# Kernel tuning notes

Measured on AMD Instinct MI355X. Metric: run time of the kernel, lower is better.

## Reference

```python
import jax, jax.numpy as jnp
import numpy as np

B, T, D, H = 4, 4096, 1024, 4
DK = D // H
DV = D // H
CH = 64           # chunk_size
C = T // CH


def setup_inputs() -> dict:
    key = jax.random.key(0)
    ks = jax.random.split(key, 10)
    def w(k, shape, fan_in):
        return jax.random.normal(k, shape, jnp.float32) * (fan_in ** -0.5)
    return {
        "x": jax.random.normal(ks[0], (B, T, D), jnp.float32),
        "Wq": w(ks[1], (D, D), D),
        "Wk": w(ks[2], (D, D), D),
        "Wv": w(ks[3], (D, D), D),
        "Wb": w(ks[4], (D, H), D),      # beta projection
        "Wa": w(ks[5], (D, H), D),      # decay-gate projection
        "A_log": jnp.log(jax.random.uniform(ks[6], (H,), jnp.float32, 1.0, 16.0)),
        "dt_bias": jnp.zeros((H,), jnp.float32),
        "Wg": w(ks[7], (D, D), D),      # output-gate projection
        "norm_w": jnp.ones((DV,), jnp.float32),
        "Wo": w(ks[8], (D, D), D),
    }


def _l2norm(x, eps=1e-6):
    return x * jax.lax.rsqrt(jnp.sum(x * x, axis=-1, keepdims=True) + eps)


def _gdn_forward(x, Wq, Wk, Wv, Wb, Wa, A_log, dt_bias, Wg, norm_w, Wo):
    # projections; q/k L2-normalized per head, q scaled by 1/sqrt(dk)
    q = _l2norm((x @ Wq).reshape(B, T, H, DK)) * (DK ** -0.5)
    k = _l2norm((x @ Wk).reshape(B, T, H, DK))
    v = (x @ Wv).reshape(B, T, H, DV)
    beta = jax.nn.sigmoid(x @ Wb)                                        # [B,T,H]
    dec = jnp.exp(-jnp.exp(A_log) * jax.nn.softplus(x @ Wa + dt_bias))   # [B,T,H] in (0,1)

    # gated delta rule recurrence: S_t = dec_t*S_{t-1} + beta_t * k_t (v_t - k_t^T S_{t-1})
    def step(S, t):
        qt, kt, vt, bt, dt = t                    # [B,H,DK],[B,H,DK],[B,H,DV],[B,H],[B,H]
        S = S * dt[..., None, None]               # gated decay of state [B,H,DK,DV]
        pred = jnp.einsum('bhk,bhkv->bhv', kt, S)
        S = S + kt[..., :, None] * (bt[..., None] * (vt - pred))[..., None, :]
        ot = jnp.einsum('bhk,bhkv->bhv', qt, S)
        return S, ot

    def chunk_fn(S, chunk):
        return jax.lax.scan(step, S, chunk)
    chunk_fn = jax.checkpoint(chunk_fn)           # store only chunk-boundary states

    def to_chunks(a):                              # [B,T,...] -> [C,CH,B,H,...]
        a = jnp.moveaxis(a, 1, 0)
        return a.reshape((C, CH) + a.shape[1:])

    xs = tuple(to_chunks(a) for a in (q, k, v, beta, dec))
    S0 = jnp.zeros((B, H, DK, DV), jnp.float32)
    _, o = jax.lax.scan(chunk_fn, S0, xs)         # o: [C,CH,B,H,DV]
    o = jnp.moveaxis(o.reshape(T, B, H, DV), 0, 1)  # [B,T,H,DV]

    # gated RMSNorm + output projection
    gate = (x @ Wg).reshape(B, T, H, DV)
    o = o * jax.lax.rsqrt(jnp.mean(o * o, axis=-1, keepdims=True) + 1e-5) * norm_w
    o = o * jax.nn.silu(gate)
    return o.reshape(B, T, D) @ Wo


def reference(x, Wq, Wk, Wv, Wb, Wa, A_log, dt_bias, Wg, norm_w, Wo):
    return _gdn_forward(x, Wq, Wk, Wv, Wb, Wa, A_log, dt_bias, Wg, norm_w, Wo)
```

## Files before the change

kernel.cpp:

```cpp
#include <hip/hip_runtime.h>

typedef unsigned short u16;
typedef __bf16 bf16x8 __attribute__((ext_vector_type(8)));
typedef u16 u16x8 __attribute__((ext_vector_type(8)));
typedef u16 u16x4 __attribute__((ext_vector_type(4)));
typedef float f32x4 __attribute__((ext_vector_type(4)));

__device__ __forceinline__ float bf2f(u16 v) {
    union { unsigned u; float f; } c; c.u = ((unsigned)v) << 16; return c.f;
}
__device__ __forceinline__ u16 f2bf_h(float f) {
    __bf16 h = (__bf16)f;
    union { __bf16 h; u16 u; } c; c.h = h; return c.u;
}

__device__ __forceinline__ bf16x8 ldfrag(const u16* base, int stride, int row0, int k0, int lane) {
    return *(const bf16x8*)(base + (size_t)(row0 + (lane & 15)) * stride + k0 + (lane >> 4) * 8);
}

__device__ __forceinline__ void block_barrier() {
    __builtin_amdgcn_sched_barrier(0);
    asm volatile("s_waitcnt lgkmcnt(0)");
    __builtin_amdgcn_s_barrier();
    __builtin_amdgcn_sched_barrier(0);
}

__device__ __forceinline__ void gl2lds16(const void* g, void* l) {
    __builtin_amdgcn_global_load_lds(
        (const __attribute__((address_space(1))) unsigned int*)g,
        (__attribute__((address_space(3))) unsigned int*)l, 16, 0, 0);
}

__global__ __launch_bounds__(256) void cvt_kernel(const float* __restrict__ src,
                                                  u16* __restrict__ dst) {
    const long i = ((long)blockIdx.x * 256 + threadIdx.x) * 4;
    f32x4 v = *(const f32x4*)(src + i);
    u16x4 o;
#pragma unroll
    for (int r = 0; r < 4; r++) o[r] = f2bf_h(v[r]);
    *(u16x4*)(dst + i) = o;
}

__global__ __launch_bounds__(256) void transpose5_kernel(const float* __restrict__ s0,
                                                         const float* __restrict__ s1,
                                                         const float* __restrict__ s2,
                                                         const float* __restrict__ s3,
                                                         const float* __restrict__ s4,
                                                         u16* __restrict__ dstBase) {
    __shared__ float tile[32][33];
    const int z = blockIdx.z;
    const float* src = (z == 0) ? s0 : (z == 1) ? s1 : (z == 2) ? s2 : (z == 3) ? s3 : s4;
    u16* dst = dstBase + (size_t)z * 1024 * 1024;
    const int n0 = blockIdx.x * 32, k0 = blockIdx.y * 32;
    const int tx = threadIdx.x, ty = threadIdx.y;
#pragma unroll
    for (int i = 0; i < 32; i += 8)
        tile[ty + i][tx] = src[(long)(k0 + ty + i) * 1024 + n0 + tx];
    __syncthreads();
#pragma unroll
    for (int i = 0; i < 32; i += 8)
        dst[(long)(n0 + ty + i) * 1024 + k0 + tx] = f2bf_h(tile[tx][ty + i]);
}

template <int F32OUT>
__global__ __launch_bounds__(256) void gemm_kernel(const u16* __restrict__ A,
                                                   const u16* __restrict__ BT,
                                                   void* __restrict__ Cv,
                                                   int M, int N, int K, int ldc) {
    __shared__ __attribute__((aligned(16))) u16 As[128][32];
    __shared__ __attribute__((aligned(16))) u16 Bs[128][32];
    const int tid  = threadIdx.x;
    const int lane = tid & 63;
    const int wave = tid >> 6;
    const int wm   = (wave >> 1) * 64;
    const int wn   = (wave & 1) * 64;
    const long m0  = (long)blockIdx.y * 128;
    const long n0  = (long)blockIdx.x * 128;

    const f32x4 zero = {0.f, 0.f, 0.f, 0.f};
    f32x4 acc[4][4];
#pragma unroll
    for (int i = 0; i < 4; i++)
#pragma unroll
        for (int j = 0; j < 4; j++) acc[i][j] = zero;

    const int r0 = tid >> 2;
    const int c0 = (tid & 3) * 8;
    const u16* Ag = A + (m0 + r0) * K + c0;
    const u16* Bg = BT + (n0 + r0) * K + c0;
    u16* AsW  = &As[wave * 16][0];
    u16* AsW2 = &As[wave * 16 + 64][0];
    u16* BsW  = &Bs[wave * 16][0];
    u16* BsW2 = &Bs[wave * 16 + 64][0];

    for (int k0 = 0; k0 < K; k0 += 32) {
        gl2lds16(Ag + k0, AsW);
        gl2lds16(Ag + (long)64 * K + k0, AsW2);
        gl2lds16(Bg + k0, BsW);
        gl2lds16(Bg + (long)64 * K + k0, BsW2);
        __syncthreads();
        const int qk = (lane >> 4) * 8;
        const int mr = lane & 15;
        bf16x8 af[4], bfr[4];
#pragma unroll
        for (int i = 0; i < 4; i++) af[i]  = *(const bf16x8*)(&As[wm + i * 16 + mr][qk]);
#pragma unroll
        for (int j = 0; j < 4; j++) bfr[j] = *(const bf16x8*)(&Bs[wn + j * 16 + mr][qk]);
#pragma unroll
        for (int i = 0; i < 4; i++)
#pragma unroll
            for (int j = 0; j < 4; j++)
                acc[i][j] = __builtin_amdgcn_mfma_f32_16x16x32_bf16(af[i], bfr[j], acc[i][j], 0, 0, 0);
        __syncthreads();
    }

    const int cr = (lane >> 4) * 4;
    const int cc = lane & 15;
#pragma unroll
    for (int i = 0; i < 4; i++) {
#pragma unroll
        for (int j = 0; j < 4; j++) {
            const long m = m0 + wm + i * 16 + cr;
            const long n = n0 + wn + j * 16 + cc;
            if (F32OUT) {
                float* C = (float*)Cv;
#pragma unroll
                for (int r = 0; r < 4; r++) C[(m + r) * ldc + n] = acc[i][j][r];
            } else {
                u16* C = (u16*)Cv;
#pragma unroll
                for (int r = 0; r < 4; r++) C[(m + r) * ldc + n] = f2bf_h(acc[i][j][r]);
            }
        }
    }
}

__global__ __launch_bounds__(1024) void norm_beta_kernel(
    const u16* __restrict__ xb, u16* __restrict__ Y,
    const float* __restrict__ Wb, const float* __restrict__ Wa,
    const float* __restrict__ A_log, const float* __restrict__ dt_bias,
    float* __restrict__ beta, float* __restrict__ dec) {
    const long row = blockIdx.x;
    const int c = threadIdx.x;
    const int h = c >> 8;
    float qv = bf2f(Y[row * 3072 + c]);
    float kv = bf2f(Y[row * 3072 + 1024 + c]);
    float xv = bf2f(xb[row * 1024 + c]);
    float vals[10];
    vals[0] = qv * qv;
    vals[1] = kv * kv;
#pragma unroll
    for (int hh = 0; hh < 4; hh++) vals[2 + hh] = xv * Wb[c * 4 + hh];
#pragma unroll
    for (int hh = 0; hh < 4; hh++) vals[6 + hh] = xv * Wa[c * 4 + hh];
#pragma unroll
    for (int i = 0; i < 10; i++)
        for (int off = 32; off; off >>= 1) vals[i] += __shfl_xor(vals[i], off, 64);

    __shared__ float wred[16][10];
    __shared__ float sQ[4], sK[4];
    const int w = c >> 6;
    if ((c & 63) == 0) {
#pragma unroll
        for (int i = 0; i < 10; i++) wred[w][i] = vals[i];
    }
    __syncthreads();
    if (c < 4) {
        float s = wred[c * 4 + 0][0] + wred[c * 4 + 1][0] + wred[c * 4 + 2][0] + wred[c * 4 + 3][0];
        sQ[c] = rsqrtf(s + 1e-6f) * 0.0625f;
    } else if (c < 8) {
        int hh = c - 4;
        float s = wred[hh * 4 + 0][1] + wred[hh * 4 + 1][1] + wred[hh * 4 + 2][1] + wred[hh * 4 + 3][1];
        sK[hh] = rsqrtf(s + 1e-6f);
    } else if (c < 12) {
        int hh = c - 8;
        float s = 0.f;
        for (int ww = 0; ww < 16; ww++) s += wred[ww][2 + hh];
        beta[row * 4 + hh] = 1.f / (1.f + expf(-s));
    } else if (c < 16) {
        int hh = c - 12;
        float s = 0.f;
        for (int ww = 0; ww < 16; ww++) s += wred[ww][6 + hh];
        float z = s + dt_bias[hh];
        float sp = (z > 0.f) ? (z + log1pf(expf(-z))) : log1pf(expf(z));
        dec[row * 4 + hh] = expf(-expf(A_log[hh]) * sp);
    }
    __syncthreads();
    Y[row * 3072 + c]        = f2bf_h(qv * sQ[h]);
    Y[row * 3072 + 1024 + c] = f2bf_h(kv * sK[h]);
}

__global__ __launch_bounds__(256) void prep_kernel(const u16* __restrict__ Y,
                                                   const float* __restrict__ beta,
                                                   const float* __restrict__ dec,
                                                   u16* __restrict__ Tg,
                                                   u16* __restrict__ Mg,
                                                   float* __restrict__ sfg) {
    __shared__ __attribute__((aligned(16))) u16 lds[38400];
    __shared__ float sf[320];
    u16* KS  = lds;
    u16* QS  = lds + 16896;
    u16* AM  = lds + 33792;
    u16* Tm  = lds;
    u16* AMT = lds + 4608;
    u16* MP  = lds + 9216;
    u16* MPT = lds + 13824;

    const int bx = blockIdx.x;
    const int bh = bx >> 6, c = bx & 63;
    const int b = bh >> 2, h = bh & 3;
    const int tid = threadIdx.x, lane = tid & 63, wv = tid >> 6;
    const int quad = lane >> 4, l15 = lane & 15;
    const int tld = tid >> 2, seg = tid & 3;
    const long bt0 = (long)b * 4096 + c * 64;
    u16* Tc = Tg + (size_t)(bh * 64 + c) * 4096;
    u16* Mc = Mg + (size_t)(bh * 64 + c) * 4096;
    const f32x4 z4 = {0.f, 0.f, 0.f, 0.f};

    {
        const long rb = (bt0 + tld) * 3072 + h * 256 + seg * 64;
#pragma unroll
        for (int i = 0; i < 8; i++) {
            *(u16x8*)&KS[tld * 264 + seg * 64 + i * 8] = *(const u16x8*)&Y[rb + 1024 + i * 8];
            *(u16x8*)&QS[tld * 264 + seg * 64 + i * 8] = *(const u16x8*)&Y[rb + i * 8];
        }
    }
    if (wv == 0) {
        float d   = dec [(bt0 + lane) * 4 + h];
        float bt_ = beta[(bt0 + lane) * 4 + h];
        float lg = log2f(fmaxf(d, 1e-30f));
#pragma unroll
        for (int off = 1; off < 64; off <<= 1) {
            float o = __shfl_up(lg, off, 64);
            if (lane >= off) lg += o;
        }
        sf[lane] = lg; sf[192 + lane] = bt_;
        float lgL = __shfl(lg, 63, 64);
        float g = exp2f(lg);
        float* sfc = sfg + (size_t)(bh * 64 + c) * 256;
        sfc[lane]       = g;
        sfc[64 + lane]  = bt_ * g;
        sfc[128 + lane] = bt_;
        sfc[192 + lane] = exp2f(lgL - lg);
    }
    __syncthreads();

    {
        const u16* Ab = (wv < 2) ? KS : QS;
        const int mb = (wv & 1) * 32;
        f32x4 g[2][4];
#pragma unroll
        for (int mi = 0; mi < 2; mi++)
#pragma unroll
            for (int sj = 0; sj < 4; sj++) g[mi][sj] = z4;
#pragma unroll 2
        for (int k0 = 0; k0 < 256; k0 += 32) {
            bf16x8 bfr[4];
#pragma unroll
            for (int sj = 0; sj < 4; sj++) bfr[sj] = ldfrag(KS, 264, sj * 16, k0, lane);
#pragma unroll
            for (int mi = 0; mi < 2; mi++) {
                bf16x8 af = ldfrag(Ab, 264, mb + mi * 16, k0, lane);
#pragma unroll
                for (int sj = 0; sj < 4; sj++)
                    g[mi][sj] = __builtin_amdgcn_mfma_f32_16x16x32_bf16(af, bfr[sj], g[mi][sj], 0, 0, 0);
            }
        }
#pragma unroll
        for (int mi = 0; mi < 2; mi++)
#pragma unroll
            for (int sj = 0; sj < 4; sj++)
#pragma unroll
                for (int r = 0; r < 4; r++) {
                    const int t_ = mb + mi * 16 + quad * 4 + r, s_ = sj * 16 + l15;
                    if (wv < 2)
                        AM[t_ * 72 + s_] = (s_ < t_) ? f2bf_h(sf[192 + t_] * exp2f(sf[t_] - sf[s_]) * g[mi][sj][r]) : (u16)0;
                    else
                        Mc[t_ * 64 + s_] = (s_ <= t_) ? f2bf_h(exp2f(sf[t_] - sf[s_]) * g[mi][sj][r]) : (u16)0;
                }
    }
    __syncthreads();

    {
        const int t_ = tid >> 2;
#pragma unroll
        for (int i = 0; i < 16; i++) {
            const int s_ = (tid & 3) * 16 + i;
            const u16 a = AM[t_ * 72 + s_];
            Tm[t_ * 72 + s_] = (t_ == s_) ? (u16)0x3F80 : (u16)(a ^ 0x8000);
            AMT[s_ * 72 + t_] = a;
        }
    }
    __syncthreads();

    {
        f32x4 sq[4];
#pragma unroll
        for (int sj = 0; sj < 4; sj++) sq[sj] = z4;
#pragma unroll
        for (int k0 = 0; k0 < 64; k0 += 32) {
            bf16x8 a = ldfrag(AM, 72, 16 * wv, k0, lane);
#pragma unroll
            for (int sj = 0; sj < 4; sj++) {
                bf16x8 bb = ldfrag(AMT, 72, sj * 16, k0, lane);
                sq[sj] = __builtin_amdgcn_mfma_f32_16x16x32_bf16(a, bb, sq[sj], 0, 0, 0);
            }
        }
#pragma unroll
        for (int sj = 0; sj < 4; sj++)
#pragma unroll
            for (int r = 0; r < 4; r++) {
                const int t_ = 16 * wv + quad * 4 + r, s_ = sj * 16 + l15;
                const u16 vbf = f2bf_h(sq[sj][r]);
                MP[t_ * 72 + s_] = vbf;
                MPT[s_ * 72 + t_] = vbf;
            }
        __syncthreads();
    }

#pragma unroll 1
    for (int jj = 0; jj < 5; jj++) {
        const bool last = (jj == 4);
        f32x4 pp[4], sq[4];
#pragma unroll
        for (int sj = 0; sj < 4; sj++) {
            sq[sj] = z4;
#pragma unroll
            for (int r = 0; r < 4; r++)
                pp[sj][r] = bf2f(Tm[(16 * wv + quad * 4 + r) * 72 + sj * 16 + l15]);
        }
#pragma unroll
        for (int k0 = 0; k0 < 64; k0 += 32) {
            bf16x8 at = ldfrag(Tm, 72, 16 * wv, k0, lane);
            bf16x8 am = ldfrag(MP, 72, 16 * wv, k0, lane);
#pragma unroll
            for (int sj = 0; sj < 4; sj++) {
                bf16x8 bb = ldfrag(MPT, 72, sj * 16, k0, lane);
                pp[sj] = __builtin_amdgcn_mfma_f32_16x16x32_bf16(at, bb, pp[sj], 0, 0, 0);
                if (!last) sq[sj] = __builtin_amdgcn_mfma_f32_16x16x32_bf16(am, bb, sq[sj], 0, 0, 0);
            }
        }
        __syncthreads();
#pragma unroll
        for (int sj = 0; sj < 4; sj++)
#pragma unroll
            for (int r = 0; r < 4; r++) {
                const int t_ = 16 * wv + quad * 4 + r, s_ = sj * 16 + l15;
                Tm[t_ * 72 + s_] = f2bf_h(pp[sj][r]);
                if (!last) {
                    const u16 vbf = f2bf_h(sq[sj][r]);
                    MP[t_ * 72 + s_] = vbf;
                    MPT[s_ * 72 + t_] = vbf;
                }
            }
        __syncthreads();
    }

    {
        const int t_ = tid >> 2;
#pragma unroll
        for (int i = 0; i < 16; i++) {
            const int s_ = (tid & 3) * 16 + i;
            Tc[t_ * 64 + s_] = Tm[t_ * 72 + s_];
        }
    }
}

struct Frag { bf16x8 f[8]; };
#define LDA 40

__global__ __launch_bounds__(512, 2) void scan_gate_kernel(
    const u16* __restrict__ Y, const float* __restrict__ sfg,
    const u16* __restrict__ Tg, const u16* __restrict__ Mg,
    u16* __restrict__ Ob,
    const float* __restrict__ x, const u16* __restrict__ WgT,
    u16* __restrict__ GX) {
    __shared__ __attribute__((aligned(16))) u16 smem[49184];

    const int tid = threadIdx.x;

    if (blockIdx.x >= 64) {
        u16* As = smem + (tid >> 8) * 9216;
        u16* Bs = As + 5120;
        const int t256 = tid & 255;
        const int lane = t256 & 63;
        const int wave = t256 >> 6;
        const int wm   = (wave >> 1) * 64;
        const int wn   = (wave & 1) * 64;
        const int tl   = (blockIdx.x - 64) * 2 + (tid >> 8);
        const long m0  = (long)(tl >> 3) * 128;
        const long n0  = (long)(tl & 7) * 128;
        const int K = 1024, ldc = 1024;

        const f32x4 zero = {0.f, 0.f, 0.f, 0.f};
        f32x4 acc[4][4];
#pragma unroll
        for (int i = 0; i < 4; i++)
#pragma unroll
            for (int j = 0; j < 4; j++) acc[i][j] = zero;

        const int r0 = t256 >> 2;
        const int c0 = (t256 & 3) * 8;
        const float* Ag = x + (m0 + r0) * K + c0;
        const u16* Bg = WgT + (n0 + r0) * K + c0;
        u16* BsW  = Bs + wave * 16 * 32;
        u16* BsW2 = Bs + (wave * 16 + 64) * 32;

        for (int k0 = 0; k0 < K; k0 += 32) {
            gl2lds16(Bg + k0, BsW);
            gl2lds16(Bg + (long)64 * K + k0, BsW2);
            f32x4 af0 = *(const f32x4*)(Ag + k0);
            f32x4 af1 = *(const f32x4*)(Ag + k0 + 4);
            f32x4 ag0 = *(const f32x4*)(Ag + (long)64 * K + k0);
            f32x4 ag1 = *(const f32x4*)(Ag + (long)64 * K + k0 + 4);
            u16x8 a0, a1;
#pragma unroll
            for (int r = 0; r < 4; r++) {
                a0[r] = f2bf_h(af0[r]); a0[r + 4] = f2bf_h(af1[r]);
                a1[r] = f2bf_h(ag0[r]); a1[r + 4] = f2bf_h(ag1[r]);
            }
            *(u16x8*)(As + r0 * LDA + c0)        = a0;
            *(u16x8*)(As + (r0 + 64) * LDA + c0) = a1;
            __syncthreads();
            const int qk = (lane >> 4) * 8;
            const int mr = lane & 15;
            bf16x8 af[4], bfr[4];
#pragma unroll
            for (int i = 0; i < 4; i++) af[i]  = *(const bf16x8*)(As + (wm + i * 16 + mr) * LDA + qk);
#pragma unroll
            for (int j = 0; j < 4; j++) bfr[j] = *(const bf16x8*)(Bs + (wn + j * 16 + mr) * 32 + qk);
#pragma unroll
            for (int i = 0; i < 4; i++)
#pragma unroll
                for (int j = 0; j < 4; j++)
                    acc[i][j] = __builtin_amdgcn_mfma_f32_16x16x32_bf16(af[i], bfr[j], acc[i][j], 0, 0, 0);
            __syncthreads();
        }

        const int cr = (lane >> 4) * 4;
        const int cc = lane & 15;
#pragma unroll
        for (int i = 0; i < 4; i++) {
#pragma unroll
            for (int j = 0; j < 4; j++) {
                const long m = m0 + wm + i * 16 + cr;
                const long n = n0 + wn + j * 16 + cc;
#pragma unroll
                for (int r = 0; r < 4; r++) GX[(m + r) * ldc + n] = f2bf_h(acc[i][j][r]);
            }
        }
        return;
    }

    u16* KT   = smem;
    u16* ST   = smem + 18464;
    u16* RHST = smem + 35360;
    u16* UTp  = smem + 39968;
    u16* UTk  = smem + 44576;

    const int px = blockIdx.x;
    const int bh = (px & 7) | ((px >> 5) << 3);
    const int dvs = (px >> 3) & 3;
    const int b = bh >> 2, h = bh & 3;
    const int lane = tid & 63, wv = tid >> 6;
    const int wq = wv & 3;
    const int isQ = wv >> 2;
    const int quad = lane >> 4, l15 = lane & 15;
    const int tW = 16 * wq + l15;
    const int tph = 16 * ((wq + quad) & 3) + l15;
    int toff[4];
#pragma unroll
    for (int j = 0; j < 4; j++) toff[j] = ((((j << 1) + (l15 >> 3)) & 3) << 4);
    const f32x4 z4 = {0.f, 0.f, 0.f, 0.f};

    f32x4 Sacc[2][4];
#pragma unroll
    for (int i = 0; i < 2; i++)
#pragma unroll
        for (int j = 0; j < 4; j++) Sacc[i][j] = z4;
    for (int i = tid; i < 64 * 264; i += 512) ST[i] = 0;
    __syncthreads();

    const long roleOff = isQ ? 0 : 1024;
    Frag F0, F1;
    {
        const u16* Pg = Y + ((long)b * 4096) * 3072 + roleOff + h * 256;
#pragma unroll
        for (int i = 0; i < 8; i++) F0.f[i] = ldfrag(Pg, 3072, 16 * wq, i * 32, lane);
    }

    f32x4 oaccP[4];
#pragma unroll
    for (int j = 0; j < 4; j++) oaccP[j] = z4;
    bf16x8 amP0 = {}, amP1 = {};
    long obP = 0;
    int havePrev = 0;

    auto body = [&](Frag& cur, Frag& nxt, int c) {
        const long bt0 = (long)b * 4096 + (long)c * 64;
        const int cn = (c < 63) ? c + 1 : 63;

        {
            const u16* Pg = Y + ((long)b * 4096 + (long)cn * 64) * 3072 + roleOff + h * 256;
#pragma unroll
            for (int i = 0; i < 8; i++) nxt.f[i] = ldfrag(Pg, 3072, 16 * wq, i * 32, lane);
        }

        const u16* Tc = Tg + (size_t)(bh * 64 + c) * 4096;
        bf16x8 at0 = ldfrag(Tc, 64, 16 * wq, 0, lane);
        bf16x8 at1 = ldfrag(Tc, 64, 16 * wq, 32, lane);
        const float* sfc = sfg + (size_t)(bh * 64 + c) * 256;
        const float gam_l = sfc[tW];
        const float bg_l  = sfc[64 + tW];
        const float bet_l = sfc[128 + tW];
        const float ksc_l = sfc[192 + tW];
        const float gL    = sfc[63];

        u16x4 v4[4];
        if (!isQ) {
            const u16* Vr = Y + (bt0 + tW) * 3072 + 2048 + h * 256 + dvs * 64;
#pragma unroll
            for (int j = 0; j < 4; j++) v4[j] = *(const u16x4*)(Vr + j * 16 + quad * 4);
        } else {
            const u16* Mc = Mg + (size_t)(bh * 64 + c) * 4096;
            bf16x8 amN0 = ldfrag(Mc, 64, 16 * wq, 0, lane);
            bf16x8 amN1 = ldfrag(Mc, 64, 16 * wq, 32, lane);
            if (havePrev) {
#pragma unroll
                for (int sj = 0; sj < 4; sj++) {
                    bf16x8 ua0 = ldfrag(UTp, 72, sj * 16, 0, lane);
                    oaccP[sj] = __builtin_amdgcn_mfma_f32_16x16x32_bf16(ua0, amP0, oaccP[sj], 0, 0, 0);
                    bf16x8 ua1 = ldfrag(UTp, 72, sj * 16, 32, lane);
                    oaccP[sj] = __builtin_amdgcn_mfma_f32_16x16x32_bf16(ua1, amP1, oaccP[sj], 0, 0, 0);
                }
#pragma unroll
                for (int sj = 0; sj < 4; sj++) {
                    u16x4 o4;
#pragma unroll
                    for (int r = 0; r < 4; r++) o4[r] = f2bf_h(oaccP[sj][r]);
                    *(u16x4*)(Ob + obP + sj * 16 + quad * 4) = o4;
                }
            }
            amP0 = amN0; amP1 = amN1;
        }

        f32x4 p[4];
#pragma unroll
        for (int j = 0; j < 4; j++) p[j] = z4;
#pragma unroll
        for (int i = 0; i < 8; i++) {
            bf16x8 sfr[4];
#pragma unroll
            for (int j = 0; j < 4; j++) sfr[j] = ldfrag(ST, 264, j * 16, i * 32, lane);
#pragma unroll
            for (int j = 0; j < 4; j++)
                p[j] = __builtin_amdgcn_mfma_f32_16x16x32_bf16(sfr[j], cur.f[i], p[j], 0, 0, 0);
        }

        if (!isQ) {
#pragma unroll
            for (int i = 0; i < 8; i++) {
                const u16* src = (const u16*)&cur.f[i];
                u16* dst = KT + (i >> 1) * 4616 + ((i & 1) * 32 + quad * 8) * 72 + tph;
#pragma unroll
                for (int jj = 0; jj < 8; jj++) dst[jj * 72] = src[jj];
            }
#pragma unroll
            for (int j = 0; j < 4; j++)
#pragma unroll
                for (int r = 0; r < 4; r++) {
                    const int row = j * 16 + quad * 4 + r;
                    RHST[row * 72 + tW] = f2bf_h(bet_l * bf2f(v4[j][r]) - bg_l * p[j][r]);
                }
        } else {
#pragma unroll
            for (int j = 0; j < 4; j++)
#pragma unroll
                for (int r = 0; r < 4; r++) oaccP[j][r] = gam_l * p[j][r];
            obP = (bt0 + tW) * 1024 + h * 256 + (long)dvs * 64;
            havePrev = 1;
        }
        block_barrier();

        {
#pragma unroll
            for (int s2 = 0; s2 < 2; s2++) {
                const int sj = isQ * 2 + s2;
                f32x4 uu = z4;
                bf16x8 ra0 = ldfrag(RHST, 72, sj * 16, 0, lane);
                uu = __builtin_amdgcn_mfma_f32_16x16x32_bf16(ra0, at0, uu, 0, 0, 0);
                bf16x8 ra1 = ldfrag(RHST, 72, sj * 16, 32, lane);
                uu = __builtin_amdgcn_mfma_f32_16x16x32_bf16(ra1, at1, uu, 0, 0, 0);
#pragma unroll
                for (int r = 0; r < 4; r++) {
                    const int row = sj * 16 + quad * 4 + r;
                    UTp[row * 72 + tW] = f2bf_h(uu[r]);
                    UTk[row * 72 + tW] = f2bf_h(ksc_l * uu[r]);
                }
            }
        }
        block_barrier();

        {
#pragma unroll
            for (int i = 0; i < 2; i++)
#pragma unroll
                for (int j = 0; j < 4; j++) Sacc[i][j] *= gL;
            const u16* KTp = KT + wq * 4616;
#pragma unroll
            for (int k0 = 0; k0 < 64; k0 += 32) {
                bf16x8 au[2], bk[4];
#pragma unroll
                for (int i = 0; i < 2; i++) au[i] = ldfrag(UTk, 72, isQ * 32 + i * 16, k0, lane);
#pragma unroll
                for (int j = 0; j < 4; j++)
                    bk[j] = *(const bf16x8*)(KTp + (size_t)(j * 16 + l15) * 72 +
                                             ((k0 + quad * 8 + toff[j]) & 63));
#pragma unroll
                for (int i = 0; i < 2; i++)
#pragma unroll
                    for (int j = 0; j < 4; j++)
                        Sacc[i][j] = __builtin_amdgcn_mfma_f32_16x16x32_bf16(au[i], bk[j], Sacc[i][j], 0, 0, 0);
            }
#pragma unroll
            for (int i = 0; i < 2; i++)
#pragma unroll
                for (int j = 0; j < 4; j++)
#pragma unroll
                    for (int r = 0; r < 4; r++)
                        ST[(isQ * 32 + i * 16 + quad * 4 + r) * 264 + wq * 64 + j * 16 + l15] = f2bf_h(Sacc[i][j][r]);
        }
        block_barrier();
    };

#pragma unroll 1
    for (int c = 0; c < 64; c += 2) {
        body(F0, F1, c);
        body(F1, F0, c + 1);
    }

    if (isQ) {
#pragma unroll
        for (int sj = 0; sj < 4; sj++) {
            bf16x8 ua0 = ldfrag(UTp, 72, sj * 16, 0, lane);
            oaccP[sj] = __builtin_amdgcn_mfma_f32_16x16x32_bf16(ua0, amP0, oaccP[sj], 0, 0, 0);
            bf16x8 ua1 = ldfrag(UTp, 72, sj * 16, 32, lane);
            oaccP[sj] = __builtin_amdgcn_mfma_f32_16x16x32_bf16(ua1, amP1, oaccP[sj], 0, 0, 0);
        }
#pragma unroll
        for (int sj = 0; sj < 4; sj++) {
            u16x4 o4;
#pragma unroll
            for (int r = 0; r < 4; r++) o4[r] = f2bf_h(oaccP[sj][r]);
            *(u16x4*)(Ob + obP + sj * 16 + quad * 4) = o4;
        }
    }
}

__global__ __launch_bounds__(256) void gate_norm_kernel(const u16* __restrict__ O,
                                                        u16* __restrict__ G,
                                                        const float* __restrict__ norm_w) {
    const long row = blockIdx.x >> 2;
    const int h = blockIdx.x & 3;
    const int dv = threadIdx.x;
    const long idx = row * 1024 + h * 256 + dv;
    float o = bf2f(O[idx]);
    float s = o * o;
#pragma unroll
    for (int off = 32; off; off >>= 1) s += __shfl_xor(s, off, 64);
    __shared__ float wsum[4];
    if ((dv & 63) == 0) wsum[dv >> 6] = s;
    __syncthreads();
    const float tot = wsum[0] + wsum[1] + wsum[2] + wsum[3];
    const float r = rsqrtf(tot * (1.f / 256.f) + 1e-5f);
    const float g = bf2f(G[idx]);
    const float val = o * r * norm_w[dv] * (g / (1.f + expf(-g)));
    G[idx] = f2bf_h(val);
}

extern "C" void kernel_launch(void* const* d_in, const int* in_sizes, int n_in,
                              void* d_out, int out_size, void* d_ws, size_t ws_size,
                              hipStream_t stream) {
    const float* x       = (const float*)d_in[0];
    const float* Wq      = (const float*)d_in[1];
    const float* Wk      = (const float*)d_in[2];
    const float* Wv      = (const float*)d_in[3];
    const float* Wb      = (const float*)d_in[4];
    const float* Wa      = (const float*)d_in[5];
    const float* A_log   = (const float*)d_in[6];
    const float* dt_bias = (const float*)d_in[7];
    const float* Wg      = (const float*)d_in[8];
    const float* norm_w  = (const float*)d_in[9];
    const float* Wo      = (const float*)d_in[10];

    char* p = (char*)d_ws;
    u16*   WT   = (u16*)p;   p += (size_t)5120 * 1024 * 2;
    u16*   Y    = (u16*)p;   p += (size_t)16384 * 3072 * 2;
    u16*   G    = (u16*)p;   p += (size_t)16384 * 1024 * 2;
    u16*   XO   = (u16*)p;   p += (size_t)16384 * 1024 * 2;
    float* beta = (float*)p; p += (size_t)16384 * 4 * 4;
    float* dec  = (float*)p; p += (size_t)16384 * 4 * 4;
    u16*   GX   = (u16*)p;   p += (size_t)16384 * 1024 * 2;

    u16* Tg = G;
    u16* Mg = G + (size_t)1024 * 4096;
    float* sfg = (float*)WT;

    cvt_kernel<<<16384, 256, 0, stream>>>(x, XO);

    transpose5_kernel<<<dim3(32, 32, 5), dim3(32, 8), 0, stream>>>(
        Wq, Wk, Wv, Wg, Wo, WT);

    gemm_kernel<0><<<dim3(3072 / 128, 16384 / 128), 256, 0, stream>>>(
        XO, WT, (void*)Y, 16384, 3072, 1024, 3072);

    norm_beta_kernel<<<16384, 1024, 0, stream>>>(XO, Y, Wb, Wa, A_log, dt_bias, beta, dec);

    prep_kernel<<<1024, 256, 0, stream>>>(Y, beta, dec, Tg, Mg, sfg);

    scan_gate_kernel<<<576, 512, 0, stream>>>(
        Y, sfg, Tg, Mg, XO, x, WT + (size_t)3072 * 1024, GX);

    gate_norm_kernel<<<16384 * 4, 256, 0, stream>>>(XO, GX, norm_w);

    gemm_kernel<1><<<dim3(1024 / 128, 16384 / 128), 256, 0, stream>>>(
        GX, WT + (size_t)4096 * 1024, d_out, 16384, 1024, 1024, 1024);
}
```

Before: 898.8 us.

## Fuse input prep kernels and compute beta/decay projections as extra GEMM column tile

Merges the x conversion and weight transpose launches into one kernel, and also builds a transposed bf16 copy of Wb/Wa. The Wa term is split into a bf16 part and a bf16 residual part to keep precision. The beta and decay pre-activations are then computed by an extra 128-column tile in the QKV GEMM instead of per-row dot-product reductions in norm_beta, so norm_beta only reduces the q/k norms. gate_norm is relaunched with one 1024-thread block per row rather than four 256-thread blocks. The extra GEMM tile wastes most of its columns and writes a 128-wide fp32 buffer per row.

```diff
diff --git a/kernel.cpp b/kernel.cpp
--- a/kernel.cpp
+++ b/kernel.cpp
@@ -31,35 +31,122 @@
         (__attribute__((address_space(3))) unsigned int*)l, 16, 0, 0);
 }
 
-__global__ __launch_bounds__(256) void cvt_kernel(const float* __restrict__ src,
-                                                  u16* __restrict__ dst) {
-    const long i = ((long)blockIdx.x * 256 + threadIdx.x) * 4;
-    f32x4 v = *(const f32x4*)(src + i);
-    u16x4 o;
-#pragma unroll
-    for (int r = 0; r < 4; r++) o[r] = f2bf_h(v[r]);
-    *(u16x4*)(dst + i) = o;
-}
-
-__global__ __launch_bounds__(256) void transpose5_kernel(const float* __restrict__ s0,
-                                                         const float* __restrict__ s1,
-                                                         const float* __restrict__ s2,
-                                                         const float* __restrict__ s3,
-                                                         const float* __restrict__ s4,
-                                                         u16* __restrict__ dstBase) {
+__global__ __launch_bounds__(256) void prep0_kernel(
+    const float* __restrict__ x, u16* __restrict__ XO,
+    const float* __restrict__ Wq, const float* __restrict__ Wk,
+    const float* __restrict__ Wv, const float* __restrict__ Wg,
+    const float* __restrict__ Wo, u16* __restrict__ WT,
+    const float* __restrict__ Wb, const float* __restrict__ Wa,
+    u16* __restrict__ WbaT) {
     __shared__ float tile[32][33];
-    const int z = blockIdx.z;
-    const float* src = (z == 0) ? s0 : (z == 1) ? s1 : (z == 2) ? s2 : (z == 3) ? s3 : s4;
-    u16* dst = dstBase + (size_t)z * 1024 * 1024;
-    const int n0 = blockIdx.x * 32, k0 = blockIdx.y * 32;
-    const int tx = threadIdx.x, ty = threadIdx.y;
-#pragma unroll
-    for (int i = 0; i < 32; i += 8)
-        tile[ty + i][tx] = src[(long)(k0 + ty + i) * 1024 + n0 + tx];
-    __syncthreads();
-#pragma unroll
-    for (int i = 0; i < 32; i += 8)
-        dst[(long)(n0 + ty + i) * 1024 + k0 + tx] = f2bf_h(tile[tx][ty + i]);
+    const int bx = blockIdx.x, tid = threadIdx.x;
+
+    if (bx < 16384) {
+        const long i = ((long)bx * 256 + tid) * 4;
+        f32x4 v = *(const f32x4*)(x + i);
+        u16x4 o;
+#pragma unroll
+        for (int r = 0; r < 4; r++) o[r] = f2bf_h(v[r]);
+        *(u16x4*)(XO + i) = o;
+        return;
+    }
+    if (bx < 21504) {
+        const int t = bx - 16384;
+        const int z = t >> 10, r = t & 1023;
+        const float* src = (z == 0) ? Wq : (z == 1) ? Wk : (z == 2) ? Wv : (z == 3) ? Wg : Wo;
+        u16* dst = WT + (size_t)z * 1024 * 1024;
+        const int n0 = (r & 31) * 32, k0 = (r >> 5) * 32;
+        const int tx = tid & 31, ty = tid >> 5;
+#pragma unroll
+        for (int i = 0; i < 32; i += 8)
+            tile[ty + i][tx] = src[(long)(k0 + ty + i) * 1024 + n0 + tx];
+        __syncthreads();
+#pragma unroll
+        for (int i = 0; i < 32; i += 8)
+            dst[(long)(n0 + ty + i) * 1024 + k0 + tx] = f2bf_h(tile[tx][ty + i]);
+        return;
+    }
+    const int t = (bx - 21504) * 256 + tid;
+    const int n = t >> 10, k = t & 1023;
+    float v;
+    if (n < 4)      v = Wb[k * 4 + n];
+    else if (n < 8) v = Wa[k * 4 + (n - 4)];
+    else { float w = Wa[k * 4 + (n - 8)]; v = w - bf2f(f2bf_h(w)); }
+    WbaT[(size_t)n * 1024 + k] = f2bf_h(v);
+}
+
+__global__ __launch_bounds__(256) void qkv_kernel(const u16* __restrict__ A,
+                                                  const u16* __restrict__ WTb,
+                                                  const u16* __restrict__ WbaT,
+                                                  u16* __restrict__ Y,
+                                                  float* __restrict__ preBA) {
+    __shared__ __attribute__((aligned(16))) u16 As[128][32];
+    __shared__ __attribute__((aligned(16))) u16 Bs[128][32];
+    const int tid  = threadIdx.x;
+    const int lane = tid & 63;
+    const int wave = tid >> 6;
+    const int wm   = (wave >> 1) * 64;
+    const int wn   = (wave & 1) * 64;
+    const int isBA = (blockIdx.x == 24);
+    const long m0  = (long)blockIdx.y * 128;
+    const long n0  = isBA ? 0 : (long)blockIdx.x * 128;
+    const u16* BT  = isBA ? WbaT : WTb;
+    const int K = 1024;
+
+    const f32x4 zero = {0.f, 0.f, 0.f, 0.f};
+    f32x4 acc[4][4];
+#pragma unroll
+    for (int i = 0; i < 4; i++)
+#pragma unroll
+        for (int j = 0; j < 4; j++) acc[i][j] = zero;
+
+    const int r0 = tid >> 2;
+    const int c0 = (tid & 3) * 8;
+    const u16* Ag = A + (m0 + r0) * K + c0;
+    const u16* Bg = BT + (n0 + r0) * K + c0;
+    u16* AsW  = &As[wave * 16][0];
+    u16* AsW2 = &As[wave * 16 + 64][0];
+    u16* BsW  = &Bs[wave * 16][0];
+    u16* BsW2 = &Bs[wave * 16 + 64][0];
+
+    for (int k0 = 0; k0 < K; k0 += 32) {
+        gl2lds16(Ag + k0, AsW);
+        gl2lds16(Ag + (long)64 * K + k0, AsW2);
+        gl2lds16(Bg + k0, BsW);
+        gl2lds16(Bg + (long)64 * K + k0, BsW2);
+        __syncthreads();
+        const int qk = (lane >> 4) * 8;
+        const int mr = lane & 15;
+        bf16x8 af[4], bfr[4];
+#pragma unroll
+        for (int i = 0; i < 4; i++) af[i]  = *(const bf16x8*)(&As[wm + i * 16 + mr][qk]);
+#pragma unroll
+        for (int j = 0; j < 4; j++) bfr[j] = *(const bf16x8*)(&Bs[wn + j * 16 + mr][qk]);
+#pragma unroll
+        for (int i = 0; i < 4; i++)
+#pragma unroll
+            for (int j = 0; j < 4; j++)
+                acc[i][j] = __builtin_amdgcn_mfma_f32_16x16x32_bf16(af[i], bfr[j], acc[i][j], 0, 0, 0);
+        __syncthreads();
+    }
+
+    const int cr = (lane >> 4) * 4;
+    const int cc = lane & 15;
+#pragma unroll
+    for (int i = 0; i < 4; i++) {
+#pragma unroll
+        for (int j = 0; j < 4; j++) {
+            const long m = m0 + wm + i * 16 + cr;
+            const long n = n0 + wn + j * 16 + cc;
+            if (isBA) {
+#pragma unroll
+                for (int r = 0; r < 4; r++) preBA[(m + r) * 128 + n] = acc[i][j][r];
+            } else {
+#pragma unroll
+                for (int r = 0; r < 4; r++) Y[(m + r) * 3072 + n] = f2bf_h(acc[i][j][r]);
+            }
+        }
+    }
 }
 
 template <int F32OUT>
@@ -136,8 +223,7 @@
 }
 
 __global__ __launch_bounds__(1024) void norm_beta_kernel(
-    const u16* __restrict__ xb, u16* __restrict__ Y,
-    const float* __restrict__ Wb, const float* __restrict__ Wa,
+    u16* __restrict__ Y, const float* __restrict__ preBA,
     const float* __restrict__ A_log, const float* __restrict__ dt_bias,
     float* __restrict__ beta, float* __restrict__ dec) {
     const long row = blockIdx.x;
@@ -145,42 +231,32 @@
     const int h = c >> 8;
     float qv = bf2f(Y[row * 3072 + c]);
     float kv = bf2f(Y[row * 3072 + 1024 + c]);
-    float xv = bf2f(xb[row * 1024 + c]);
-    float vals[10];
-    vals[0] = qv * qv;
-    vals[1] = kv * kv;
-#pragma unroll
-    for (int hh = 0; hh < 4; hh++) vals[2 + hh] = xv * Wb[c * 4 + hh];
-#pragma unroll
-    for (int hh = 0; hh < 4; hh++) vals[6 + hh] = xv * Wa[c * 4 + hh];
-#pragma unroll
-    for (int i = 0; i < 10; i++)
-        for (int off = 32; off; off >>= 1) vals[i] += __shfl_xor(vals[i], off, 64);
-
-    __shared__ float wred[16][10];
+    float s0 = qv * qv;
+    float s1 = kv * kv;
+#pragma unroll
+    for (int off = 32; off; off >>= 1) {
+        s0 += __shfl_xor(s0, off, 64);
+        s1 += __shfl_xor(s1, off, 64);
+    }
+    __shared__ float wq_[16], wk_[16];
     __shared__ float sQ[4], sK[4];
     const int w = c >> 6;
-    if ((c & 63) == 0) {
-#pragma unroll
-        for (int i = 0; i < 10; i++) wred[w][i] = vals[i];
-    }
+    if ((c & 63) == 0) { wq_[w] = s0; wk_[w] = s1; }
     __syncthreads();
     if (c < 4) {
-        float s = wred[c * 4 + 0][0] + wred[c * 4 + 1][0] + wred[c * 4 + 2][0] + wred[c * 4 + 3][0];
+        float s = wq_[c * 4] + wq_[c * 4 + 1] + wq_[c * 4 + 2] + wq_[c * 4 + 3];
         sQ[c] = rsqrtf(s + 1e-6f) * 0.0625f;
     } else if (c < 8) {
         int hh = c - 4;
-        float s = wred[hh * 4 + 0][1] + wred[hh * 4 + 1][1] + wred[hh * 4 + 2][1] + wred[hh * 4 + 3][1];
+        float s = wk_[hh * 4] + wk_[hh * 4 + 1] + wk_[hh * 4 + 2] + wk_[hh * 4 + 3];
         sK[hh] = rsqrtf(s + 1e-6f);
     } else if (c < 12) {
         int hh = c - 8;
-        float s = 0.f;
-        for (int ww = 0; ww < 16; ww++) s += wred[ww][2 + hh];
+        float s = preBA[row * 128 + hh];
         beta[row * 4 + hh] = 1.f / (1.f + expf(-s));
     } else if (c < 16) {
         int hh = c - 12;
-        float s = 0.f;
-        for (int ww = 0; ww < 16; ww++) s += wred[ww][6 + hh];
+        float s = preBA[row * 128 + 4 + hh] + preBA[row * 128 + 8 + hh];
         float z = s + dt_bias[hh];
         float sp = (z > 0.f) ? (z + log1pf(expf(-z))) : log1pf(expf(z));
         dec[row * 4 + hh] = expf(-expf(A_log[hh]) * sp);
@@ -657,21 +733,22 @@
     }
 }
 
-__global__ __launch_bounds__(256) void gate_norm_kernel(const u16* __restrict__ O,
-                                                        u16* __restrict__ G,
-                                                        const float* __restrict__ norm_w) {
-    const long row = blockIdx.x >> 2;
-    const int h = blockIdx.x & 3;
-    const int dv = threadIdx.x;
-    const long idx = row * 1024 + h * 256 + dv;
+__global__ __launch_bounds__(1024) void gate_norm_kernel(const u16* __restrict__ O,
+                                                         u16* __restrict__ G,
+                                                         const float* __restrict__ norm_w) {
+    const long row = blockIdx.x;
+    const int c = threadIdx.x;
+    const int h = c >> 8;
+    const int dv = c & 255;
+    const long idx = row * 1024 + c;
     float o = bf2f(O[idx]);
     float s = o * o;
 #pragma unroll
     for (int off = 32; off; off >>= 1) s += __shfl_xor(s, off, 64);
-    __shared__ float wsum[4];
-    if ((dv & 63) == 0) wsum[dv >> 6] = s;
+    __shared__ float wsum[16];
+    if ((c & 63) == 0) wsum[c >> 6] = s;
     __syncthreads();
-    const float tot = wsum[0] + wsum[1] + wsum[2] + wsum[3];
+    const float tot = wsum[h * 4] + wsum[h * 4 + 1] + wsum[h * 4 + 2] + wsum[h * 4 + 3];
     const float r = rsqrtf(tot * (1.f / 256.f) + 1e-5f);
     const float g = bf2f(G[idx]);
     const float val = o * r * norm_w[dv] * (g / (1.f + expf(-g)));
@@ -695,33 +772,31 @@
 
     char* p = (char*)d_ws;
     u16*   WT   = (u16*)p;   p += (size_t)5120 * 1024 * 2;
+    u16*   WbaT = (u16*)p;   p += (size_t)128 * 1024 * 2;
     u16*   Y    = (u16*)p;   p += (size_t)16384 * 3072 * 2;
     u16*   G    = (u16*)p;   p += (size_t)16384 * 1024 * 2;
     u16*   XO   = (u16*)p;   p += (size_t)16384 * 1024 * 2;
     float* beta = (float*)p; p += (size_t)16384 * 4 * 4;
     float* dec  = (float*)p; p += (size_t)16384 * 4 * 4;
     u16*   GX   = (u16*)p;   p += (size_t)16384 * 1024 * 2;
+    float* preBA = (float*)p; p += (size_t)16384 * 128 * 4;
 
     u16* Tg = G;
     u16* Mg = G + (size_t)1024 * 4096;
     float* sfg = (float*)WT;
 
-    cvt_kernel<<<16384, 256, 0, stream>>>(x, XO);
-
-    transpose5_kernel<<<dim3(32, 32, 5), dim3(32, 8), 0, stream>>>(
-        Wq, Wk, Wv, Wg, Wo, WT);
-
-    gemm_kernel<0><<<dim3(3072 / 128, 16384 / 128), 256, 0, stream>>>(
-        XO, WT, (void*)Y, 16384, 3072, 1024, 3072);
-
-    norm_beta_kernel<<<16384, 1024, 0, stream>>>(XO, Y, Wb, Wa, A_log, dt_bias, beta, dec);
+    prep0_kernel<<<21552, 256, 0, stream>>>(x, XO, Wq, Wk, Wv, Wg, Wo, WT, Wb, Wa, WbaT);
+
+    qkv_kernel<<<dim3(25, 16384 / 128), 256, 0, stream>>>(XO, WT, WbaT, Y, preBA);
+
+    norm_beta_kernel<<<16384, 1024, 0, stream>>>(Y, preBA, A_log, dt_bias, beta, dec);
 
     prep_kernel<<<1024, 256, 0, stream>>>(Y, beta, dec, Tg, Mg, sfg);
 
     scan_gate_kernel<<<576, 512, 0, stream>>>(
         Y, sfg, Tg, Mg, XO, x, WT + (size_t)3072 * 1024, GX);
 
-    gate_norm_kernel<<<16384 * 4, 256, 0, stream>>>(XO, GX, norm_w);
+    gate_norm_kernel<<<16384, 1024, 0, stream>>>(XO, GX, norm_w);
 
     gemm_kernel<1><<<dim3(1024 / 128, 16384 / 128), 256, 0, stream>>>(
         GX, WT + (size_t)4096 * 1024, d_out, 16384, 1024, 1024, 1024);
```

Measured after the change: 861.0 us. 4.2% less time.
